# Optimization experiments

Measured on AMD Instinct MI355X. Metric: run time of the kernel, lower is better.

## Reference

```python
import jax, jax.numpy as jnp
import numpy as np

NUM_HEADS = 8


def _layernorm(x, w, b, eps=1e-5):
    # normalize over last axis (channels)
    mu = jnp.mean(x, axis=-1, keepdims=True)
    var = jnp.var(x, axis=-1, keepdims=True)
    return (x - mu) * jax.lax.rsqrt(var + eps) * w + b


def setup_inputs() -> dict:
    key = jax.random.key(0)
    ks = jax.random.split(key, 5)
    B, C, H, W = 8, 512, 32, 32
    x = jax.random.normal(ks[0], (B, C, H, W), dtype=jnp.float32)
    ln_w = jnp.ones((C,), dtype=jnp.float32)
    ln_b = jnp.zeros((C,), dtype=jnp.float32)
    qkv_w = jax.random.normal(ks[1], (3 * C, C), dtype=jnp.float32) * (1.0 / np.sqrt(C))
    qkv_b = jax.random.normal(ks[2], (3 * C,), dtype=jnp.float32) * 0.02
    proj_w = jax.random.normal(ks[3], (C, C), dtype=jnp.float32) * (1.0 / np.sqrt(C))
    proj_b = jax.random.normal(ks[4], (C,), dtype=jnp.float32) * 0.02
    return {"x": x, "ln_w": ln_w, "ln_b": ln_b, "qkv_w": qkv_w,
            "qkv_b": qkv_b, "proj_w": proj_w, "proj_b": proj_b}


def reference(x, ln_w, ln_b, qkv_w, qkv_b, proj_w, proj_b):
    B, C, H, W = x.shape
    nh = NUM_HEADS
    hd = C // nh
    HW = H * W
    residual = x
    # LayerNorm over channels: (B,C,H,W) -> (B,H,W,C)
    xn = _layernorm(x.transpose(0, 2, 3, 1), ln_w, ln_b)  # (B,H,W,C)
    # 1x1 conv == per-pixel linear: (B,H,W,3C)
    qkv = jnp.einsum('bhwc,oc->bhwo', xn, qkv_w) + qkv_b
    # match torch reshape (B,3,nh,hd,HW).permute(1,0,2,4,3)
    qkv = qkv.reshape(B, HW, 3, nh, hd).transpose(2, 0, 3, 1, 4)  # (3,B,nh,HW,hd)
    q, k, v = qkv[0], qkv[1], qkv[2]
    scale = 1.0 / jnp.sqrt(jnp.asarray(hd, dtype=x.dtype))
    attn = jnp.einsum('bnqd,bnkd->bnqk', q, k) * scale  # (B,nh,HW,HW)
    attn = jax.nn.softmax(attn, axis=-1)
    out = jnp.einsum('bnqk,bnkd->bnqd', attn, v)  # (B,nh,HW,hd)
    out = out.transpose(0, 2, 1, 3).reshape(B, H, W, C)
    out = jnp.einsum('bhwc,oc->bhwo', out, proj_w) + proj_b
    return out.transpose(0, 3, 1, 2) + residual
```

## Files before the change

kernel.cpp:

```cpp
#include <hip/hip_runtime.h>

typedef __bf16 bf16;
typedef __bf16 bf16x8 __attribute__((ext_vector_type(8)));
typedef float f32x4 __attribute__((ext_vector_type(4)));

#define MFMA16(a, b, c) __builtin_amdgcn_mfma_f32_16x16x32_bf16(a, b, c, 0, 0, 0)

#define QSCALE 0.1803368801111137f

static __device__ __forceinline__ unsigned int pack2(float a, float b) {
  unsigned short s0 = __builtin_bit_cast(unsigned short, (bf16)a);
  unsigned short s1 = __builtin_bit_cast(unsigned short, (bf16)b);
  return (unsigned int)s0 | ((unsigned int)s1 << 16);
}

static __device__ __forceinline__ void gl16(const bf16* g, bf16* l) {
  __builtin_amdgcn_global_load_lds(
      (const __attribute__((address_space(1))) unsigned int*)g,
      (__attribute__((address_space(3))) unsigned int*)l, 16, 0, 0);
}

__global__ __launch_bounds__(256) void convert_w(const float* __restrict__ qkvw,
                                                 const float* __restrict__ projw,
                                                 bf16* __restrict__ wc) {
  int c4 = blockIdx.x * 256 + threadIdx.x;
  const float* src = (c4 < 196608) ? (qkvw + (size_t)c4 * 4)
                                   : (projw + (size_t)(c4 - 196608) * 4);
  float4 v = *(const float4*)src;
  uint2 o;
  o.x = pack2(v.x, v.y);
  o.y = pack2(v.z, v.w);
  *(uint2*)&wc[(size_t)c4 * 4] = o;
}

__global__ __launch_bounds__(256) void ln_kernel(const float* __restrict__ x,
                                                 const float* __restrict__ lnw,
                                                 const float* __restrict__ lnb,
                                                 bf16* __restrict__ xn) {
  __shared__ float tile[512 * 17];
  __shared__ float wsh[512];
  __shared__ float bsh[512];
  const int t = threadIdx.x;
  const int b = blockIdx.x >> 6;
  const int p0 = (blockIdx.x & 63) * 16;
  for (int i = t; i < 512; i += 256) {
    wsh[i] = lnw[i];
    bsh[i] = lnb[i];
  }
  const float* xb = x + (size_t)b * 524288 + p0;
#pragma unroll
  for (int i = 0; i < 8; ++i) {
    int chunk = t + 256 * i;
    int c = chunk >> 2, px4 = (chunk & 3) * 4;
    float4 v = *(const float4*)&xb[(size_t)c * 1024 + px4];
    tile[c * 17 + px4 + 0] = v.x;
    tile[c * 17 + px4 + 1] = v.y;
    tile[c * 17 + px4 + 2] = v.z;
    tile[c * 17 + px4 + 3] = v.w;
  }
  __syncthreads();
  const int pix = t >> 4, j = t & 15;
  float sum = 0.f, sq = 0.f;
#pragma unroll
  for (int i = 0; i < 32; ++i) {
    int c = i * 16 + j;
    float v = tile[c * 17 + pix];
    sum += v;
    sq += v * v;
  }
#pragma unroll
  for (int m = 1; m <= 8; m <<= 1) {
    sum += __shfl_xor(sum, m);
    sq += __shfl_xor(sq, m);
  }
  float mu = sum * (1.f / 512.f);
  float var = sq * (1.f / 512.f) - mu * mu;
  float rstd = rsqrtf(var + 1e-5f);
  unsigned int* orow =
      (unsigned int*)(xn + ((size_t)(b * 1024 + p0 + pix)) * 512);
#pragma unroll
  for (int i = 0; i < 16; ++i) {
    int dw = i * 16 + j;
    int c0 = 2 * dw, c1 = 2 * dw + 1;
    float v0 = (tile[c0 * 17 + pix] - mu) * rstd * wsh[c0] + bsh[c0];
    float v1 = (tile[c1 * 17 + pix] - mu) * rstd * wsh[c1] + bsh[c1];
    orow[dw] = pack2(v0, v1);
  }
}

__global__ __launch_bounds__(256, 3) void gemm_qkv(
    const bf16* __restrict__ A, const bf16* __restrict__ Bm,
    const float* __restrict__ bias, bf16* __restrict__ oq,
    bf16* __restrict__ okk, bf16* __restrict__ ov) {
  __shared__ bf16 smem[16384];
  bf16* ash = smem;
  bf16* bsh = smem + 8192;
  const int t = threadIdx.x;
  const int lane = t & 63, w = t >> 6;
  const int quad = lane >> 4, r16 = lane & 15;
  const int wm = w >> 1, wn = w & 1;
  const int pid = blockIdx.x;
  const int panel = pid / 96, within = pid % 96;
  const int m0 = (panel * 8 + (within & 7)) * 128;
  const int n0 = (within >> 3) * 128;
  int soff[4];
  int sr[4];
#pragma unroll
  for (int j = 0; j < 4; ++j) {
    int c = (w * 4 + j) * 64 + lane;
    int r = c >> 3, cc = c & 7;
    sr[j] = r;
    soff[j] = (cc ^ (r & 7)) * 8;
  }
  f32x4 acc[4][4] = {};
  for (int k0 = 0; k0 < 512; k0 += 64) {
#pragma unroll
    for (int j = 0; j < 4; ++j) {
      gl16(&A[(size_t)(m0 + sr[j]) * 512 + k0 + soff[j]],
           &ash[(w * 4 + j) * 512]);
      gl16(&Bm[(size_t)(n0 + sr[j]) * 512 + k0 + soff[j]],
           &bsh[(w * 4 + j) * 512]);
    }
    __syncthreads();
#pragma unroll
    for (int kc = 0; kc < 2; ++kc) {
      bf16x8 af[4], bfr[4];
#pragma unroll
      for (int i = 0; i < 4; ++i) {
        int row = wm * 64 + i * 16 + r16;
        af[i] = *(const bf16x8*)&ash[row * 64 +
                                     ((kc * 4 + quad) ^ (r16 & 7)) * 8];
      }
#pragma unroll
      for (int i = 0; i < 4; ++i) {
        int row = wn * 64 + i * 16 + r16;
        bfr[i] = *(const bf16x8*)&bsh[row * 64 +
                                      ((kc * 4 + quad) ^ (r16 & 7)) * 8];
      }
#pragma unroll
      for (int tm = 0; tm < 4; ++tm)
#pragma unroll
        for (int tn = 0; tn < 4; ++tn)
          acc[tm][tn] = MFMA16(af[tm], bfr[tn], acc[tm][tn]);
    }
    __syncthreads();
  }
  if (n0 < 1024) {
#pragma unroll
    for (int tm = 0; tm < 4; ++tm) {
#pragma unroll
      for (int tn = 0; tn < 4; ++tn) {
        int n = n0 + wn * 64 + tn * 16 + r16;
        float bn = bias[n];
        int comp = n >> 9, h = (n >> 6) & 7, d = n & 63;
#pragma unroll
        for (int r = 0; r < 4; ++r) {
          int m = m0 + wm * 64 + tm * 16 + quad * 4 + r;
          float v = acc[tm][tn][r] + bn;
          int b = m >> 10, p = m & 1023;
          size_t base = ((size_t)(b * 8 + h)) * 65536;
          if (comp == 0)
            oq[base + (size_t)p * 64 + d] = (bf16)(v * QSCALE);
          else
            okk[base + (size_t)p * 64 + d] = (bf16)v;
        }
      }
    }
  } else {
    bf16* tb = &smem[w * 4096];
#pragma unroll
    for (int tn = 0; tn < 4; ++tn) {
      int n = n0 + wn * 64 + tn * 16 + r16;
      float bn = bias[n];
      int row = tn * 16 + r16;
#pragma unroll
      for (int tm = 0; tm < 4; ++tm) {
        f32x4 a = acc[tm][tn];
        uint2 pk;
        pk.x = pack2(a[0] + bn, a[1] + bn);
        pk.y = pack2(a[2] + bn, a[3] + bn);
        int g = (tm * 2 + (quad >> 1)) ^ (row & 7);
        *(uint2*)&tb[row * 64 + g * 8 + (quad & 1) * 4] = pk;
      }
    }
    const int h = ((n0 - 1024) >> 6) + wn;
    const int mw = m0 + wm * 64;
    const int b = mw >> 10;
    bf16* vbase = ov + ((size_t)(b * 8 + h)) * 65536 + (mw & 1023);
#pragma unroll
    for (int pass = 0; pass < 8; ++pass) {
      int row = pass * 8 + (lane >> 3);
      int g = (lane & 7) ^ (row & 7);
      uint4 vd = *(uint4*)&tb[row * 64 + g * 8];
      *(uint4*)&vbase[(size_t)row * 1024 + (lane & 7) * 8] = vd;
    }
  }
}

__global__ __launch_bounds__(256, 4) void gemm_proj(
    const bf16* __restrict__ Wm, const bf16* __restrict__ A,
    const float* __restrict__ bias, const float* __restrict__ resid,
    float* __restrict__ op) {
  __shared__ bf16 ash[2][64 * 64];
  __shared__ bf16 bsh[2][64 * 64];
  const int t = threadIdx.x;
  const int lane = t & 63, w = t >> 6;
  const int quad = lane >> 4, r16 = lane & 15;
  const int wm = w >> 1, wn = w & 1;
  const int m0 = blockIdx.x * 64, n0 = blockIdx.y * 64;
  int soff[2], sr[2];
#pragma unroll
  for (int j = 0; j < 2; ++j) {
    int c = (w * 2 + j) * 64 + lane;
    int r = c >> 3, cc = c & 7;
    sr[j] = r;
    soff[j] = (cc ^ (r & 7)) * 8;
  }
  f32x4 acc[2][2] = {};
#pragma unroll
  for (int j = 0; j < 2; ++j) {
    gl16(&Wm[(size_t)(m0 + sr[j]) * 512 + soff[j]], &ash[0][(w * 2 + j) * 512]);
    gl16(&A[(size_t)(n0 + sr[j]) * 512 + soff[j]], &bsh[0][(w * 2 + j) * 512]);
  }
  __syncthreads();
  for (int it = 0; it < 8; ++it) {
    const int cur = it & 1, nxt = cur ^ 1;
    if (it < 7) {
      int k1 = (it + 1) * 64;
#pragma unroll
      for (int j = 0; j < 2; ++j) {
        gl16(&Wm[(size_t)(m0 + sr[j]) * 512 + k1 + soff[j]],
             &ash[nxt][(w * 2 + j) * 512]);
        gl16(&A[(size_t)(n0 + sr[j]) * 512 + k1 + soff[j]],
             &bsh[nxt][(w * 2 + j) * 512]);
      }
    }
#pragma unroll
    for (int kc = 0; kc < 2; ++kc) {
      bf16x8 af[2], bfr[2];
#pragma unroll
      for (int i = 0; i < 2; ++i) {
        int row = wm * 32 + i * 16 + r16;
        af[i] = *(const bf16x8*)&ash[cur][row * 64 +
                                          ((kc * 4 + quad) ^ (r16 & 7)) * 8];
      }
#pragma unroll
      for (int i = 0; i < 2; ++i) {
        int row = wn * 32 + i * 16 + r16;
        bfr[i] = *(const bf16x8*)&bsh[cur][row * 64 +
                                           ((kc * 4 + quad) ^ (r16 & 7)) * 8];
      }
#pragma unroll
      for (int tm = 0; tm < 2; ++tm)
#pragma unroll
        for (int tn = 0; tn < 2; ++tn)
          acc[tm][tn] = MFMA16(af[tm], bfr[tn], acc[tm][tn]);
    }
    __syncthreads();
  }
#pragma unroll
  for (int tm = 0; tm < 2; ++tm) {
#pragma unroll
    for (int tn = 0; tn < 2; ++tn) {
      int n = n0 + wn * 32 + tn * 16 + r16;
      int b = n >> 10, p = n & 1023;
#pragma unroll
      for (int r = 0; r < 4; ++r) {
        int m = m0 + wm * 32 + tm * 16 + quad * 4 + r;
        size_t idx = ((size_t)(b * 512 + m)) * 1024 + p;
        op[idx] = acc[tm][tn][r] + bias[m] + resid[idx];
      }
    }
  }
}

__global__ __launch_bounds__(256, 4) void attn_kernel(
    const bf16* __restrict__ q, const bf16* __restrict__ k,
    const bf16* __restrict__ vT, bf16* __restrict__ o) {
  __shared__ bf16 kt[2][64 * 64];
  __shared__ bf16 vt[2][64 * 64];
  __shared__ bf16 psh[4][16 * 40];
  const int t = threadIdx.x;
  const int lane = t & 63, w = t >> 6;
  const int quad = lane >> 4, r16 = lane & 15;
  const int bh = blockIdx.x;
  const int qt0 = blockIdx.y * 64;
  const bf16* qb = q + (size_t)bh * 65536;
  const bf16* kb = k + (size_t)bh * 65536;
  const bf16* vb = vT + (size_t)bh * 65536;
  const int qrow = qt0 + w * 16 + r16;
  bf16x8 qf0 = *(const bf16x8*)&qb[(size_t)qrow * 64 + quad * 8];
  bf16x8 qf1 = *(const bf16x8*)&qb[(size_t)qrow * 64 + 32 + quad * 8];
  int offk[2], offv[2];
#pragma unroll
  for (int j = 0; j < 2; ++j) {
    int c = (w * 2 + j) * 64 + lane;
    int r = c >> 3, cc = c & 7;
    int sw = (cc ^ (r & 7)) * 8;
    offk[j] = r * 64 + sw;
    offv[j] = r * 1024 + sw;
  }
  f32x4 rsum = {};
  f32x4 oacc[4] = {};
  bf16* pw = psh[w];
  const int swz = r16 & 7;
#pragma unroll
  for (int j = 0; j < 2; ++j) {
    gl16(&kb[offk[j]], &kt[0][(w * 2 + j) * 512]);
    gl16(&vb[offv[j]], &vt[0][(w * 2 + j) * 512]);
  }
  __syncthreads();
  for (int it = 0; it < 16; ++it) {
    const int cur = it & 1, nxt = cur ^ 1;
    if (it < 15) {
      int kv1 = (it + 1) * 64;
#pragma unroll
      for (int j = 0; j < 2; ++j) {
        gl16(&kb[(size_t)kv1 * 64 + offk[j]], &kt[nxt][(w * 2 + j) * 512]);
        gl16(&vb[(size_t)kv1 + offv[j]], &vt[nxt][(w * 2 + j) * 512]);
      }
    }
    const bf16* ktc = kt[cur];
    const bf16* vtc = vt[cur];
    f32x4 s[4];
#pragma unroll
    for (int tn = 0; tn < 4; ++tn) {
      const bf16* kr = &ktc[(tn * 16 + r16) * 64];
      bf16x8 kf0 = *(const bf16x8*)&kr[(quad ^ swz) * 8];
      bf16x8 kf1 = *(const bf16x8*)&kr[((4 + quad) ^ swz) * 8];
      f32x4 z = {};
      z = MFMA16(qf0, kf0, z);
      z = MFMA16(qf1, kf1, z);
      s[tn] = z;
    }
#pragma unroll
    for (int tn = 0; tn < 4; ++tn)
#pragma unroll
      for (int r = 0; r < 4; ++r) {
        float p = __builtin_exp2f(s[tn][r]);
        s[tn][r] = p;
        rsum[r] += p;
      }
#pragma unroll
    for (int kc = 0; kc < 2; ++kc) {
#pragma unroll
      for (int tt = 0; tt < 2; ++tt)
#pragma unroll
        for (int r = 0; r < 4; ++r)
          pw[(quad * 4 + r) * 40 + tt * 16 + r16] = (bf16)s[kc * 2 + tt][r];
      bf16x8 pf = *(const bf16x8*)&pw[r16 * 40 + quad * 8];
#pragma unroll
      for (int tn = 0; tn < 4; ++tn) {
        const bf16* vr = &vtc[(tn * 16 + r16) * 64];
        bf16x8 vf = *(const bf16x8*)&vr[((kc * 4 + quad) ^ swz) * 8];
        oacc[tn] = MFMA16(pf, vf, oacc[tn]);
      }
    }
    __syncthreads();
  }
#pragma unroll
  for (int msk = 1; msk <= 8; msk <<= 1)
#pragma unroll
    for (int r = 0; r < 4; ++r) rsum[r] += __shfl_xor(rsum[r], msk);
  float inv[4];
#pragma unroll
  for (int r = 0; r < 4; ++r) inv[r] = 1.f / rsum[r];
  const int b = bh >> 3, h = bh & 7;
#pragma unroll
  for (int tn = 0; tn < 4; ++tn)
#pragma unroll
    for (int r = 0; r < 4; ++r) {
      int p = qt0 + w * 16 + quad * 4 + r;
      o[((size_t)(b * 1024 + p)) * 512 + h * 64 + tn * 16 + r16] =
          (bf16)(oacc[tn][r] * inv[r]);
    }
}

extern "C" void kernel_launch(void* const* d_in, const int* in_sizes, int n_in,
                              void* d_out, int out_size, void* d_ws,
                              size_t ws_size, hipStream_t stream) {
  (void)in_sizes;
  (void)n_in;
  (void)out_size;
  (void)ws_size;
  const float* x = (const float*)d_in[0];
  const float* lnw = (const float*)d_in[1];
  const float* lnb = (const float*)d_in[2];
  const float* qkvw = (const float*)d_in[3];
  const float* qkvb = (const float*)d_in[4];
  const float* projw = (const float*)d_in[5];
  const float* projb = (const float*)d_in[6];
  float* out = (float*)d_out;

  const size_t NELEM = 4194304;
  bf16* wc = (bf16*)d_ws;
  bf16* xn = wc + 1048576;
  bf16* qws = xn + NELEM;
  bf16* kws = qws + NELEM;
  bf16* vws = kws + NELEM;
  bf16* aws = xn;

  convert_w<<<dim3(1024), dim3(256), 0, stream>>>(qkvw, projw, wc);
  ln_kernel<<<dim3(512), dim3(256), 0, stream>>>(x, lnw, lnb, xn);
  gemm_qkv<<<dim3(768), dim3(256), 0, stream>>>(xn, wc, qkvb, qws, kws, vws);
  attn_kernel<<<dim3(64, 16), dim3(256), 0, stream>>>(qws, kws, vws, aws);
  gemm_proj<<<dim3(8, 128), dim3(256), 0, stream>>>(wc + 786432, aws, projb, x,
                                                    out);
}
```

Before: 154.7 us.

## Triple-buffer K/V and GEMM tiles with a single vmcnt-wait barrier per step

Both the attention kernel and the projection GEMM move from double-buffered LDS tiles with two __syncthreads per iteration to a three-stage ring. Each step issues the next tile's global_load_lds, waits on vmcnt for the current tile, and uses one s_barrier. The aim is to cut barrier stalls and keep more loads in flight. In exchange the larger LDS footprint lowers occupancy to 3 blocks per CU, and the P scratch row stride shrinks from 40 to 36, which may misalign the 16-byte LDS reads.

```diff
diff --git a/kernel.cpp b/kernel.cpp
--- a/kernel.cpp
+++ b/kernel.cpp
@@ -7,6 +7,9 @@
 #define MFMA16(a, b, c) __builtin_amdgcn_mfma_f32_16x16x32_bf16(a, b, c, 0, 0, 0)
 
 #define QSCALE 0.1803368801111137f
+
+#define WAITVM_BARRIER(N) \
+  asm volatile("s_waitcnt vmcnt(" #N ")\n\ts_barrier" ::: "memory")
 
 static __device__ __forceinline__ unsigned int pack2(float a, float b) {
   unsigned short s0 = __builtin_bit_cast(unsigned short, (bf16)a);
@@ -197,12 +200,12 @@
   }
 }
 
-__global__ __launch_bounds__(256, 4) void gemm_proj(
+__global__ __launch_bounds__(256, 3) void gemm_proj(
     const bf16* __restrict__ Wm, const bf16* __restrict__ A,
     const float* __restrict__ bias, const float* __restrict__ resid,
     float* __restrict__ op) {
-  __shared__ bf16 ash[2][64 * 64];
-  __shared__ bf16 bsh[2][64 * 64];
+  __shared__ bf16 ash[3][4096];
+  __shared__ bf16 bsh[3][4096];
   const int t = threadIdx.x;
   const int lane = t & 63, w = t >> 6;
   const int quad = lane >> 4, r16 = lane & 15;
@@ -217,37 +220,29 @@
     soff[j] = (cc ^ (r & 7)) * 8;
   }
   f32x4 acc[2][2] = {};
-#pragma unroll
-  for (int j = 0; j < 2; ++j) {
-    gl16(&Wm[(size_t)(m0 + sr[j]) * 512 + soff[j]], &ash[0][(w * 2 + j) * 512]);
-    gl16(&A[(size_t)(n0 + sr[j]) * 512 + soff[j]], &bsh[0][(w * 2 + j) * 512]);
-  }
-  __syncthreads();
-  for (int it = 0; it < 8; ++it) {
-    const int cur = it & 1, nxt = cur ^ 1;
-    if (it < 7) {
-      int k1 = (it + 1) * 64;
-#pragma unroll
-      for (int j = 0; j < 2; ++j) {
-        gl16(&Wm[(size_t)(m0 + sr[j]) * 512 + k1 + soff[j]],
-             &ash[nxt][(w * 2 + j) * 512]);
-        gl16(&A[(size_t)(n0 + sr[j]) * 512 + k1 + soff[j]],
-             &bsh[nxt][(w * 2 + j) * 512]);
-      }
-    }
+  auto stage = [&](int k0, int buf) {
+#pragma unroll
+    for (int j = 0; j < 2; ++j) {
+      gl16(&Wm[(size_t)(m0 + sr[j]) * 512 + k0 + soff[j]],
+           &ash[buf][(w * 2 + j) * 512]);
+      gl16(&A[(size_t)(n0 + sr[j]) * 512 + k0 + soff[j]],
+           &bsh[buf][(w * 2 + j) * 512]);
+    }
+  };
+  auto compute = [&](int buf) {
 #pragma unroll
     for (int kc = 0; kc < 2; ++kc) {
       bf16x8 af[2], bfr[2];
 #pragma unroll
       for (int i = 0; i < 2; ++i) {
         int row = wm * 32 + i * 16 + r16;
-        af[i] = *(const bf16x8*)&ash[cur][row * 64 +
+        af[i] = *(const bf16x8*)&ash[buf][row * 64 +
                                           ((kc * 4 + quad) ^ (r16 & 7)) * 8];
       }
 #pragma unroll
       for (int i = 0; i < 2; ++i) {
         int row = wn * 32 + i * 16 + r16;
-        bfr[i] = *(const bf16x8*)&bsh[cur][row * 64 +
+        bfr[i] = *(const bf16x8*)&bsh[buf][row * 64 +
                                            ((kc * 4 + quad) ^ (r16 & 7)) * 8];
       }
 #pragma unroll
@@ -256,8 +251,19 @@
         for (int tn = 0; tn < 2; ++tn)
           acc[tm][tn] = MFMA16(af[tm], bfr[tn], acc[tm][tn]);
     }
-    __syncthreads();
-  }
+  };
+  stage(0, 0);
+  int cur = 0;
+  for (int it = 0; it < 7; ++it) {
+    int nxt = cur + 1;
+    if (nxt == 3) nxt = 0;
+    stage((it + 1) * 64, nxt);
+    WAITVM_BARRIER(4);
+    compute(cur);
+    cur = nxt;
+  }
+  WAITVM_BARRIER(0);
+  compute(cur);
 #pragma unroll
   for (int tm = 0; tm < 2; ++tm) {
 #pragma unroll
@@ -274,12 +280,12 @@
   }
 }
 
-__global__ __launch_bounds__(256, 4) void attn_kernel(
+__global__ __launch_bounds__(256, 3) void attn_kernel(
     const bf16* __restrict__ q, const bf16* __restrict__ k,
     const bf16* __restrict__ vT, bf16* __restrict__ o) {
-  __shared__ bf16 kt[2][64 * 64];
-  __shared__ bf16 vt[2][64 * 64];
-  __shared__ bf16 psh[4][16 * 40];
+  __shared__ bf16 kt[3][4096];
+  __shared__ bf16 vt[3][4096];
+  __shared__ bf16 psh[4][16 * 36];
   const int t = threadIdx.x;
   const int lane = t & 63, w = t >> 6;
   const int quad = lane >> 4, r16 = lane & 15;
@@ -304,24 +310,17 @@
   f32x4 oacc[4] = {};
   bf16* pw = psh[w];
   const int swz = r16 & 7;
-#pragma unroll
-  for (int j = 0; j < 2; ++j) {
-    gl16(&kb[offk[j]], &kt[0][(w * 2 + j) * 512]);
-    gl16(&vb[offv[j]], &vt[0][(w * 2 + j) * 512]);
-  }
-  __syncthreads();
-  for (int it = 0; it < 16; ++it) {
-    const int cur = it & 1, nxt = cur ^ 1;
-    if (it < 15) {
-      int kv1 = (it + 1) * 64;
-#pragma unroll
-      for (int j = 0; j < 2; ++j) {
-        gl16(&kb[(size_t)kv1 * 64 + offk[j]], &kt[nxt][(w * 2 + j) * 512]);
-        gl16(&vb[(size_t)kv1 + offv[j]], &vt[nxt][(w * 2 + j) * 512]);
-      }
-    }
-    const bf16* ktc = kt[cur];
-    const bf16* vtc = vt[cur];
+  auto stage = [&](int tile, int buf) {
+    size_t kv = (size_t)tile * 64;
+#pragma unroll
+    for (int j = 0; j < 2; ++j) {
+      gl16(&kb[kv * 64 + offk[j]], &kt[buf][(w * 2 + j) * 512]);
+      gl16(&vb[kv + offv[j]], &vt[buf][(w * 2 + j) * 512]);
+    }
+  };
+  auto compute = [&](int buf) {
+    const bf16* ktc = kt[buf];
+    const bf16* vtc = vt[buf];
     f32x4 s[4];
 #pragma unroll
     for (int tn = 0; tn < 4; ++tn) {
@@ -347,8 +346,8 @@
       for (int tt = 0; tt < 2; ++tt)
 #pragma unroll
         for (int r = 0; r < 4; ++r)
-          pw[(quad * 4 + r) * 40 + tt * 16 + r16] = (bf16)s[kc * 2 + tt][r];
-      bf16x8 pf = *(const bf16x8*)&pw[r16 * 40 + quad * 8];
+          pw[(quad * 4 + r) * 36 + tt * 16 + r16] = (bf16)s[kc * 2 + tt][r];
+      bf16x8 pf = *(const bf16x8*)&pw[r16 * 36 + quad * 8];
 #pragma unroll
       for (int tn = 0; tn < 4; ++tn) {
         const bf16* vr = &vtc[(tn * 16 + r16) * 64];
@@ -356,8 +355,19 @@
         oacc[tn] = MFMA16(pf, vf, oacc[tn]);
       }
     }
-    __syncthreads();
-  }
+  };
+  stage(0, 0);
+  int cur = 0;
+  for (int it = 0; it < 15; ++it) {
+    int nxt = cur + 1;
+    if (nxt == 3) nxt = 0;
+    stage(it + 1, nxt);
+    WAITVM_BARRIER(4);
+    compute(cur);
+    cur = nxt;
+  }
+  WAITVM_BARRIER(0);
+  compute(cur);
 #pragma unroll
   for (int msk = 1; msk <= 8; msk <<= 1)
 #pragma unroll
```

Result: slower. 167.6 us (+8.4%).
